# Kernel optimization log

Hardware: AMD Instinct MI355X
Metric: run time of the kernel (lower is better)

## Reference

```python
import jax, jax.numpy as jnp
import numpy as np

B, S, D, H, FFN = 8, 1024, 1024, 16, 4096
DH = D // H  # per-head dim = 64
NEG = -1e9
EPS = 1e-5


def layer_norm(x):
    # F.layer_norm over last dim, no affine params (matches add_and_norm_dropout)
    mu = jnp.mean(x, axis=-1, keepdims=True)
    var = jnp.var(x, axis=-1, keepdims=True)
    return (x - mu) / jnp.sqrt(var + EPS)


def setup_inputs() -> dict:
    key = jax.random.key(0)
    ks = jax.random.split(key, 10)
    scale = 1.0 / np.sqrt(D)
    x = jax.random.normal(ks[0], (B, S, D), dtype=jnp.float32)
    real_lengths = jax.random.randint(ks[1], (B,), 1, S + 1)
    # per-head projection weights stacked: [H, D, DH] (nn.Linear(D, DH, bias=False) per head)
    Wq = jax.random.uniform(ks[2], (H, D, DH), jnp.float32, -scale, scale)
    Wk = jax.random.uniform(ks[3], (H, D, DH), jnp.float32, -scale, scale)
    Wv = jax.random.uniform(ks[4], (H, D, DH), jnp.float32, -scale, scale)
    Wo = jax.random.uniform(ks[5], (D, H * DH), jnp.float32, -scale, scale)  # Linear(H*DH, D, bias=False)
    W1 = jax.random.uniform(ks[6], (FFN, D), jnp.float32, -scale, scale)
    b1 = jax.random.uniform(ks[7], (FFN,), jnp.float32, -scale, scale)
    s2 = 1.0 / np.sqrt(FFN)
    W2 = jax.random.uniform(ks[8], (D, FFN), jnp.float32, -s2, s2)
    b2 = jax.random.uniform(ks[9], (D,), jnp.float32, -s2, s2)
    return {"x": x, "real_lengths": real_lengths, "Wq": Wq, "Wk": Wk, "Wv": Wv,
            "Wo": Wo, "W1": W1, "b1": b1, "W2": W2, "b2": b2}


def reference(x, real_lengths, Wq, Wk, Wv, Wo, W1, b1, W2, b2):
    b, s, d = x.shape
    # padding mask: True where key position >= real_length (masked out)
    key_pad = jnp.arange(s)[None, :] >= real_lengths[:, None]  # [B, S]

    # batched per-head projections (equivalent to the Python per-head loop)
    q = jnp.einsum('bsd,hde->bhse', x, Wq)
    k = jnp.einsum('bsd,hde->bhse', x, Wk)
    v = jnp.einsum('bsd,hde->bhse', x, Wv)

    scores = jnp.einsum('bhse,bhte->bhst', q, k) / jnp.sqrt(jnp.float32(DH))
    scores = jnp.where(key_pad[:, None, None, :], NEG, scores)
    attn = jax.nn.softmax(scores, axis=-1)
    heads = jnp.einsum('bhst,bhte->bhse', attn, v)       # [B,H,S,DH]
    concat = heads.transpose(0, 2, 1, 3).reshape(b, s, d)  # head concat
    attn_out = concat @ Wo.T

    x1 = layer_norm(x + attn_out)  # add & norm (eval: no dropout)

    ffn = jax.nn.relu(x1 @ W1.T + b1) @ W2.T + b2
    return layer_norm(x1 + ffn)
```

## Files before the change

### kernel.cpp

```cpp
#include <hip/hip_runtime.h>
#include <hip/hip_bf16.h>
#include <math.h>

#define B_ 8
#define S_ 1024
#define D_ 1024
#define H_ 16
#define DH_ 64
#define FFN_ 4096
#define NEG_ (-1e9f)
#define EPS_ 1e-5f

typedef float f32x4 __attribute__((ext_vector_type(4)));
typedef short bf16x8 __attribute__((ext_vector_type(8)));

__device__ __forceinline__ ushort f2b(float f) {
  __hip_bfloat16 h = __float2bfloat16(f);
  return *reinterpret_cast<ushort*>(&h);
}
__device__ __forceinline__ float b2f(ushort u) {
  return __uint_as_float((unsigned)u << 16);
}

__device__ __forceinline__ void gload16(const void* g, void* l) {
  auto* lp = (__attribute__((address_space(3))) unsigned*)(uintptr_t)(l);
  __builtin_amdgcn_global_load_lds(
      (const __attribute__((address_space(1))) unsigned*)g, lp, 16, 0, 0);
}

__device__ __forceinline__ void* swz_ptr(void* base, int row, int col) {
  int byte = (row << 7) + (col << 1);
  byte ^= (row & 7) << 4;
  return (char*)base + byte;
}

__global__ __launch_bounds__(256) void prep_k(
    const float* __restrict__ x, const float* __restrict__ Wq,
    const float* __restrict__ Wk, const float* __restrict__ Wv,
    const float* __restrict__ Wo, const float* __restrict__ W1,
    const float* __restrict__ W2, ushort* __restrict__ xbf,
    ushort* __restrict__ qkvw, ushort* __restrict__ wob,
    ushort* __restrict__ w1b, ushort* __restrict__ w2b) {
  const int blk = blockIdx.x, t = threadIdx.x;
  if (blk < 8192) {
    int i = blk * 256 + t;
    float4 v = ((const float4*)x)[i];
    ushort4 o;
    o.x = f2b(v.x); o.y = f2b(v.y); o.z = f2b(v.z); o.w = f2b(v.w);
    ((ushort4*)xbf)[i] = o;
  } else if (blk < 8192 + 12288) {
    int idx = (blk - 8192) * 256 + t;
    int e = idx & 63, k = (idx >> 6) & 1023;
    int h = (idx >> 16) & 15, which = idx >> 20;
    const float* W = (which == 0) ? Wq : (which == 1 ? Wk : Wv);
    float v = W[((size_t)h * D_ + k) * DH_ + e];
    qkvw[((size_t)which * 1024 + h * 64 + e) * 1024 + k] = f2b(v);
  } else if (blk < 8192 + 12288 + 1024) {
    int i = (blk - 8192 - 12288) * 256 + t;
    float4 v = ((const float4*)Wo)[i];
    ushort4 o;
    o.x = f2b(v.x); o.y = f2b(v.y); o.z = f2b(v.z); o.w = f2b(v.w);
    ((ushort4*)wob)[i] = o;
  } else if (blk < 8192 + 12288 + 1024 + 4096) {
    int i = (blk - 8192 - 12288 - 1024) * 256 + t;
    float4 v = ((const float4*)W1)[i];
    ushort4 o;
    o.x = f2b(v.x); o.y = f2b(v.y); o.z = f2b(v.z); o.w = f2b(v.w);
    ((ushort4*)w1b)[i] = o;
  } else {
    int i = (blk - 8192 - 12288 - 1024 - 4096) * 256 + t;
    float4 v = ((const float4*)W2)[i];
    ushort4 o;
    o.x = f2b(v.x); o.y = f2b(v.y); o.z = f2b(v.z); o.w = f2b(v.w);
    ((ushort4*)w2b)[i] = o;
  }
}

template <int BIAS, int RELU, int OUT_BF16, int VSPLIT>
__global__ __launch_bounds__(256) void gemm_bf16(
    const ushort* __restrict__ A, const ushort* __restrict__ Bt,
    const float* __restrict__ bias, void* __restrict__ C,
    ushort* __restrict__ vT, int M, int N, int K) {
  __shared__ ushort Al[2][128 * 64];
  __shared__ ushort Bl[2][128 * 64];
  const int nb = N >> 7;
  const int bm = blockIdx.x / nb, bn = blockIdx.x % nb;
  const int t = threadIdx.x;
  const int lane = t & 63;
  const int wid = t >> 6, wr = wid >> 1, wc = wid & 1;
  const int row0 = bm << 7, col0 = bn << 7;
  const size_t Kb = (size_t)K * 2;
  const int NT = K >> 6;

  const char* Abase = (const char*)A + (size_t)row0 * Kb;
  const char* Bbase = (const char*)Bt + (size_t)col0 * Kb;

  f32x4 acc[4][4] = {};
  const int o0 = t * 16;
  const int lrow = lane & 15, lkb = (lane >> 4) * 8;

  auto STAGE = [&](int buf, int kt) {
#pragma unroll
    for (int i = 0; i < 4; i++) {
      int ob = o0 + i * 4096;
      int row = ob >> 7, inrow = ob & 127;
      const char* ga = Abase + (size_t)row * Kb + kt * 128 + inrow;
      const char* gb = Bbase + (size_t)row * Kb + kt * 128 + inrow;
      gload16(ga, (char*)&Al[buf][0] + ob);
      gload16(gb, (char*)&Bl[buf][0] + ob);
    }
  };
  auto COMPUTE = [&](int buf) {
#pragma unroll
    for (int kk = 0; kk < 64; kk += 32) {
      bf16x8 af[4], bfr[4];
      const int lk = lkb + kk;
#pragma unroll
      for (int m = 0; m < 4; m++)
        af[m] = *(const bf16x8*)&Al[buf][(wr * 64 + m * 16 + lrow) * 64 + lk];
#pragma unroll
      for (int n = 0; n < 4; n++)
        bfr[n] = *(const bf16x8*)&Bl[buf][(wc * 64 + n * 16 + lrow) * 64 + lk];
#pragma unroll
      for (int m = 0; m < 4; m++)
#pragma unroll
        for (int n = 0; n < 4; n++)
          acc[m][n] = __builtin_amdgcn_mfma_f32_16x16x32_bf16(
              af[m], bfr[n], acc[m][n], 0, 0, 0);
    }
  };

  STAGE(0, 0);
  __syncthreads();
  int cur = 0;
  for (int kt = 1; kt < NT; kt++) {
    STAGE(cur ^ 1, kt);
    COMPUTE(cur);
    __syncthreads();
    cur ^= 1;
  }
  COMPUTE(cur);

  const int rbase = row0 + wr * 64 + (lane >> 4) * 4;
  const int cbase = col0 + wc * 64 + (lane & 15);
#pragma unroll
  for (int m = 0; m < 4; m++) {
#pragma unroll
    for (int n = 0; n < 4; n++) {
      int col = cbase + n * 16;
      float bv = BIAS ? bias[col] : 0.0f;
      if (VSPLIT && col >= 2048) {
        int row = rbase + m * 16;
        int hh = (col - 2048) >> 6, e = col & 63;
        ushort4 uv;
        uv.x = f2b(acc[m][n][0]); uv.y = f2b(acc[m][n][1]);
        uv.z = f2b(acc[m][n][2]); uv.w = f2b(acc[m][n][3]);
        *(ushort4*)&vT[((((size_t)(row >> 10) * 16 + hh) * 64 + e) << 10) +
                       (row & 1023)] = uv;
      } else {
#pragma unroll
        for (int q = 0; q < 4; q++) {
          int row = rbase + m * 16 + q;
          float v = acc[m][n][q] + bv;
          if (RELU) v = fmaxf(v, 0.0f);
          if (VSPLIT) {
            ((ushort*)C)[(size_t)row * 2048 + col] = f2b(v);
          } else if (OUT_BF16) {
            ((ushort*)C)[(size_t)row * N + col] = f2b(v);
          } else {
            ((float*)C)[(size_t)row * N + col] = v;
          }
        }
      }
    }
  }
}

__global__ __launch_bounds__(256) void attention_mfma_k(
    const ushort* __restrict__ qk, const ushort* __restrict__ vT,
    const int* __restrict__ lens, ushort* __restrict__ concat) {
  __shared__ ushort Qs[64 * 64];
  __shared__ ushort Ks[64 * 64];
  __shared__ ushort Vt[64 * 64];
  __shared__ ushort Pl[4][16 * 64];
  const int blk = blockIdx.x;
  const int b = blk & 7, h = (blk >> 3) & 15, q0 = (blk >> 7) << 6;
  const int t = threadIdx.x;
  const int lane = t & 63, w = t >> 6;
  const int lr = lane & 15, lg = lane >> 4;
  const int lg4 = lg * 4;
  const int len_b = lens[b];
  ushort* Plw = &Pl[w][0];
  const ushort* vbase = vT + ((size_t)(b * 16 + h) << 16);

#pragma unroll
  for (int i = 0; i < 4; i++) {
    int idx = t + i * 256;
    int r = idx >> 4, eq = idx & 15;
    const ushort* src =
        qk + ((size_t)(b * S_ + q0 + r)) * 2048 + h * 64 + eq * 4;
    *(ushort4*)swz_ptr(Qs, r, eq * 4) = *(const ushort4*)src;
  }
  __syncthreads();
  bf16x8 qf[2];
#pragma unroll
  for (int ds = 0; ds < 2; ds++)
    qf[ds] = *(const bf16x8*)swz_ptr(Qs, w * 16 + lr, lg * 8 + ds * 32);

  float mrun = -INFINITY, lrun = 0.f;
  f32x4 o[4] = {};

  ushort4 kreg[4], vreg[4];
  auto LOADT = [&](int j0) {
#pragma unroll
    for (int i = 0; i < 4; i++) {
      int idx = t + i * 256;
      int r = idx >> 4, eq = idx & 15;
      kreg[i] = *(const ushort4*)(qk + ((size_t)(b * S_ + j0 + r)) * 2048 +
                                  1024 + h * 64 + eq * 4);
      vreg[i] = *(const ushort4*)(vbase + (size_t)r * 1024 + j0 + eq * 4);
    }
  };

  const int ntiles = (len_b + 63) >> 6;
  LOADT(0);
  for (int jt = 0; jt < ntiles; jt++) {
    const int j0 = jt << 6;
    __syncthreads();
#pragma unroll
    for (int i = 0; i < 4; i++) {
      int idx = t + i * 256;
      int r = idx >> 4, eq = idx & 15;
      *(ushort4*)swz_ptr(Ks, r, eq * 4) = kreg[i];
      *(ushort4*)swz_ptr(Vt, r, eq * 4) = vreg[i];
    }
    if (jt + 1 < ntiles) LOADT(j0 + 64);
    __syncthreads();

    f32x4 sacc[4];
    __builtin_amdgcn_s_setprio(1);
#pragma unroll
    for (int mb = 0; mb < 4; mb++) {
      sacc[mb] = (f32x4){0.f, 0.f, 0.f, 0.f};
#pragma unroll
      for (int ds = 0; ds < 2; ds++) {
        bf16x8 kf = *(const bf16x8*)swz_ptr(Ks, mb * 16 + lr, lg * 8 + ds * 32);
        sacc[mb] = __builtin_amdgcn_mfma_f32_16x16x32_bf16(kf, qf[ds], sacc[mb],
                                                           0, 0, 0);
      }
    }
    __builtin_amdgcn_s_setprio(0);

    float p[4][4];
    float pmax = -INFINITY;
#pragma unroll
    for (int mb = 0; mb < 4; mb++)
#pragma unroll
      for (int qi = 0; qi < 4; qi++) {
        float v = sacc[mb][qi] * 0.125f;
        if (j0 + mb * 16 + lg4 + qi >= len_b) v = NEG_;
        p[mb][qi] = v;
        pmax = fmaxf(pmax, v);
      }
    pmax = fmaxf(pmax, __shfl_xor(pmax, 16));
    pmax = fmaxf(pmax, __shfl_xor(pmax, 32));
    if (!__all(pmax - mrun <= 8.0f)) {
      float mnew = fmaxf(mrun, pmax);
      float sc = __expf(mrun - mnew);
      mrun = mnew;
      lrun *= sc;
#pragma unroll
      for (int qi = 0; qi < 4; qi++) {
        float scq = __shfl(sc, (lg << 4) + lg4 + qi);
#pragma unroll
        for (int dt = 0; dt < 4; dt++) o[dt][qi] *= scq;
      }
    }
    float rs = 0.f;
#pragma unroll
    for (int mb = 0; mb < 4; mb++)
#pragma unroll
      for (int qi = 0; qi < 4; qi++) {
        float e = __expf(p[mb][qi] - mrun);
        p[mb][qi] = e;
        rs += e;
      }
    rs += __shfl_xor(rs, 16);
    rs += __shfl_xor(rs, 32);
    lrun += rs;

#pragma unroll
    for (int mb = 0; mb < 4; mb++) {
      ushort2 w0, w1;
      w0.x = f2b(p[mb][0]); w0.y = f2b(p[mb][1]);
      w1.x = f2b(p[mb][2]); w1.y = f2b(p[mb][3]);
      *(ushort2*)swz_ptr(Plw, lr, mb * 16 + lg4) = w0;
      *(ushort2*)swz_ptr(Plw, lr, mb * 16 + lg4 + 2) = w1;
    }

    bf16x8 pf[2];
#pragma unroll
    for (int ks = 0; ks < 2; ks++)
      pf[ks] = *(const bf16x8*)swz_ptr(Plw, lr, lg * 8 + ks * 32);
    __builtin_amdgcn_s_setprio(1);
#pragma unroll
    for (int dt = 0; dt < 4; dt++) {
#pragma unroll
      for (int ks = 0; ks < 2; ks++) {
        bf16x8 vf = *(const bf16x8*)swz_ptr(Vt, dt * 16 + lr, lg * 8 + ks * 32);
        o[dt] = __builtin_amdgcn_mfma_f32_16x16x32_bf16(pf[ks], vf, o[dt],
                                                        0, 0, 0);
      }
    }
    __builtin_amdgcn_s_setprio(0);
  }

#pragma unroll
  for (int qi = 0; qi < 4; qi++) {
    float lq = __shfl(lrun, (lg << 4) + lg4 + qi);
    float inv = 1.0f / lq;
    size_t row = (size_t)(b * S_ + q0 + w * 16 + lg4 + qi);
#pragma unroll
    for (int dt = 0; dt < 4; dt++)
      concat[row * 1024 + h * 64 + dt * 16 + lr] = f2b(o[dt][qi] * inv);
  }
}

template <int WBF>
__global__ __launch_bounds__(256) void add_ln_k(const float* __restrict__ a,
                                                const ushort* __restrict__ r,
                                                float* __restrict__ y,
                                                ushort* __restrict__ yb) {
  const int row = blockIdx.x, t = threadIdx.x;
  const float4 av = ((const float4*)(a + (size_t)row * 1024))[t];
  const ushort4 rv = ((const ushort4*)(r + (size_t)row * 1024))[t];
  float v[4] = {av.x + b2f(rv.x), av.y + b2f(rv.y), av.z + b2f(rv.z),
                av.w + b2f(rv.w)};
  float s = v[0] + v[1] + v[2] + v[3];
  float q = v[0] * v[0] + v[1] * v[1] + v[2] * v[2] + v[3] * v[3];
#pragma unroll
  for (int off = 1; off < 64; off <<= 1) {
    s += __shfl_xor(s, off);
    q += __shfl_xor(q, off);
  }
  __shared__ float ss[4], sq[4];
  int wave = t >> 6, lane = t & 63;
  if (lane == 0) { ss[wave] = s; sq[wave] = q; }
  __syncthreads();
  s = ss[0] + ss[1] + ss[2] + ss[3];
  q = sq[0] + sq[1] + sq[2] + sq[3];
  float mean = s * (1.f / 1024.f);
  float var = q * (1.f / 1024.f) - mean * mean;
  float inv = 1.0f / sqrtf(var + EPS_);
  float4 yo;
  yo.x = (v[0] - mean) * inv; yo.y = (v[1] - mean) * inv;
  yo.z = (v[2] - mean) * inv; yo.w = (v[3] - mean) * inv;
  ((float4*)(y + (size_t)row * 1024))[t] = yo;
  if (WBF) {
    ushort4 ob;
    ob.x = f2b(yo.x); ob.y = f2b(yo.y); ob.z = f2b(yo.z); ob.w = f2b(yo.w);
    ((ushort4*)(yb + (size_t)row * 1024))[t] = ob;
  }
}

extern "C" void kernel_launch(void* const* d_in, const int* in_sizes, int n_in,
                              void* d_out, int out_size, void* d_ws, size_t ws_size,
                              hipStream_t stream) {
  const float* x  = (const float*)d_in[0];
  const int* len  = (const int*)d_in[1];
  const float* Wq = (const float*)d_in[2];
  const float* Wk = (const float*)d_in[3];
  const float* Wv = (const float*)d_in[4];
  const float* Wo = (const float*)d_in[5];
  const float* W1 = (const float*)d_in[6];
  const float* b1 = (const float*)d_in[7];
  const float* W2 = (const float*)d_in[8];
  const float* b2 = (const float*)d_in[9];
  float* out = (float*)d_out;

  if (ws_size < (size_t)184 * 1024 * 1024) return;
  char* w = (char*)d_ws;
  ushort* xbf    = (ushort*)(w);
  ushort* qkvw   = (ushort*)(w + ((size_t)16 << 20));
  ushort* wob    = (ushort*)(w + ((size_t)22 << 20));
  ushort* w1b    = (ushort*)(w + ((size_t)24 << 20));
  ushort* w2b    = (ushort*)(w + ((size_t)32 << 20));
  ushort* qk2    = (ushort*)(w + ((size_t)40 << 20));
  ushort* vT     = (ushort*)(w + ((size_t)72 << 20));
  ushort* concat = (ushort*)(w + ((size_t)88 << 20));
  ushort* attno  = (ushort*)(w + ((size_t)104 << 20));
  float*  x1     = (float*) (w + ((size_t)136 << 20));
  ushort* x1b    = (ushort*)(w + ((size_t)168 << 20));
  ushort* hidden = (ushort*)(w + ((size_t)40 << 20));
  ushort* ffn2o  = (ushort*)(w + ((size_t)104 << 20));

  prep_k<<<29696, 256, 0, stream>>>(x, Wq, Wk, Wv, Wo, W1, W2,
                                    xbf, qkvw, wob, w1b, w2b);

  gemm_bf16<0, 0, 1, 1><<<64 * 24, 256, 0, stream>>>(xbf, qkvw, nullptr, qk2,
                                                     vT, 8192, 3072, 1024);
  attention_mfma_k<<<2048, 256, 0, stream>>>(qk2, vT, len, concat);
  gemm_bf16<0, 0, 1, 0><<<64 * 8, 256, 0, stream>>>(concat, wob, nullptr,
                                                    attno, nullptr,
                                                    8192, 1024, 1024);
  add_ln_k<1><<<8192, 256, 0, stream>>>(x, attno, x1, x1b);
  gemm_bf16<1, 1, 1, 0><<<64 * 32, 256, 0, stream>>>(x1b, w1b, b1, hidden,
                                                     nullptr, 8192, 4096, 1024);
  gemm_bf16<1, 0, 1, 0><<<64 * 8, 256, 0, stream>>>(hidden, w2b, b2, ffn2o,
                                                    nullptr, 8192, 1024, 4096);
  add_ln_k<0><<<8192, 256, 0, stream>>>(x1, ffn2o, out, nullptr);
}
```

Baseline: 404.0 us.

## Add 256x256 8-wave ping-pong GEMM for QKV and FFN1 projections

Adds a new GEMM kernel that uses 256x256 output tiles, 512 threads (8 waves), split-K-half LDS staging with double buffering, explicit barriers and waitcnts, MFMA priority boosting, and an XCD-aware block swizzle. It replaces the old 128x128 kernel for the wide QKV (N=3072) and FFN1 (N=4096) GEMMs, aiming for more data reuse per tile and better overlap of global loads with MFMA work. The old kernel is simplified and kept for the N=1024 GEMMs. The risks are fewer workgroups (384 and 512), which may underfill the CUs, higher register pressure from 32 accumulators per lane, and fragile hand-written synchronisation.

Measured after the change: 386.2 us. 1.05x faster.

```diff
diff --git a/kernel.cpp b/kernel.cpp
--- a/kernel.cpp
+++ b/kernel.cpp
@@ -33,6 +33,13 @@
   byte ^= (row & 7) << 4;
   return (char*)base + byte;
 }
+
+#define BARR asm volatile("s_barrier" ::: "memory")
+#define LGKM0                                         \
+  do {                                                \
+    asm volatile("s_waitcnt lgkmcnt(0)" ::: "memory"); \
+    __builtin_amdgcn_sched_barrier(0);                \
+  } while (0)
 
 __global__ __launch_bounds__(256) void prep_k(
     const float* __restrict__ x, const float* __restrict__ Wq,
@@ -76,11 +83,144 @@
   }
 }
 
-template <int BIAS, int RELU, int OUT_BF16, int VSPLIT>
+template <int BIAS, int RELU, int VSPLIT>
+__global__ __launch_bounds__(512, 2) void gemm8p(
+    const ushort* __restrict__ A, const ushort* __restrict__ Bt,
+    const float* __restrict__ bias, ushort* __restrict__ C,
+    ushort* __restrict__ vT, int M, int N, int K) {
+  __shared__ ushort lds[2][2][2][256 * 32];
+  const int nbn = N >> 8;
+  const int nwg = gridDim.x;
+  const int cpx = nwg >> 3;
+  const int bid = blockIdx.x;
+  const int swz = (bid & 7) * cpx + (bid >> 3);
+  const int bm = swz / nbn, bn = swz % nbn;
+
+  const int t = threadIdx.x;
+  const int lane = t & 63, lr = lane & 15, lg = lane >> 4;
+  const int wid = t >> 6, wr = wid >> 2, wc = wid & 3;
+  const size_t Kb = (size_t)K * 2;
+  const char* Ab = (const char*)A + ((size_t)(bm << 8)) * Kb;
+  const char* Bb = (const char*)Bt + ((size_t)(bn << 8)) * Kb;
+  const int NT = K >> 6;
+  const int niter = NT >> 1;
+
+  const int g0row = t >> 2;
+  const int gsi = (t & 3) ^ (g0row & 3);
+  auto STG = [&](int mat, int kh, int kt) {
+    char* base = (char*)&lds[kt & 1][mat][kh][0];
+    const char* gsrc = mat ? Bb : Ab;
+#pragma unroll
+    for (int j = 0; j < 2; j++) {
+      int row = g0row + j * 128;
+      const char* src = gsrc + (size_t)row * Kb +
+                        (size_t)(kt * 64 + kh * 32) * 2 + gsi * 16;
+      gload16(src, base + t * 16 + j * 8192);
+    }
+  };
+
+  const int rg = (lg ^ (lr & 3)) << 3;
+#define LDA(DST, BUF, KH, QM)                                            \
+  _Pragma("unroll") for (int mm = 0; mm < 4; mm++) {                     \
+    int row = wr * 128 + (QM)*64 + mm * 16 + lr;                         \
+    DST[mm] = *(const bf16x8*)&lds[BUF][0][KH][row * 32 + rg];           \
+  }
+#define LDB(DST, BUF, KH)                                                \
+  _Pragma("unroll") for (int nn = 0; nn < 4; nn++) {                     \
+    int row = wc * 64 + nn * 16 + lr;                                    \
+    DST[nn] = *(const bf16x8*)&lds[BUF][1][KH][row * 32 + rg];           \
+  }
+#define MFQ(QM, AS, BS)                                                  \
+  do {                                                                   \
+    __builtin_amdgcn_s_setprio(1);                                       \
+    _Pragma("unroll") for (int mm = 0; mm < 4; mm++)                     \
+        _Pragma("unroll") for (int nn = 0; nn < 4; nn++)                 \
+            acc[(QM)*4 + mm][nn] = __builtin_amdgcn_mfma_f32_16x16x32_bf16( \
+                AS[mm], BS[nn], acc[(QM)*4 + mm][nn], 0, 0, 0);          \
+    __builtin_amdgcn_s_setprio(0);                                       \
+  } while (0)
+
+  f32x4 acc[8][4] = {};
+  bf16x8 aS0[4], aS1[4], bS0[4], bS1[4];
+
+  STG(0, 0, 0); STG(1, 0, 0); STG(0, 1, 0); STG(1, 1, 0);
+  STG(0, 0, 1); STG(1, 0, 1);
+  asm volatile("s_waitcnt vmcnt(4)" ::: "memory");
+  BARR;
+
+  for (int i = 0; i < niter; i++) {
+    const int c1 = 2 * i + 1, c2 = 2 * i + 2, c3 = 2 * i + 3;
+    LDA(aS0, 0, 0, 0); LDB(bS0, 0, 0); STG(0, 1, c1);
+    BARR; LGKM0; MFQ(0, aS0, bS0); BARR;
+    LDA(aS1, 0, 0, 1); STG(1, 1, c1);
+    BARR; LGKM0; MFQ(1, aS1, bS0); BARR;
+    LDA(aS0, 0, 1, 0); LDB(bS1, 0, 1);
+    if (c2 < NT) STG(0, 0, c2);
+    BARR; LGKM0; MFQ(0, aS0, bS1); BARR;
+    LDA(aS1, 0, 1, 1);
+    if (c2 < NT) STG(1, 0, c2);
+    BARR; LGKM0; MFQ(1, aS1, bS1);
+    if (i + 1 < niter)
+      asm volatile("s_waitcnt vmcnt(4)" ::: "memory");
+    else
+      asm volatile("s_waitcnt vmcnt(0)" ::: "memory");
+    BARR;
+    LDA(aS0, 1, 0, 0); LDB(bS0, 1, 0);
+    if (c2 < NT) STG(0, 1, c2);
+    BARR; LGKM0; MFQ(0, aS0, bS0); BARR;
+    LDA(aS1, 1, 0, 1);
+    if (c2 < NT) STG(1, 1, c2);
+    BARR; LGKM0; MFQ(1, aS1, bS0); BARR;
+    LDA(aS0, 1, 1, 0); LDB(bS1, 1, 1);
+    if (c3 < NT) STG(0, 0, c3);
+    BARR; LGKM0; MFQ(0, aS0, bS1); BARR;
+    LDA(aS1, 1, 1, 1);
+    if (c3 < NT) STG(1, 0, c3);
+    BARR; LGKM0; MFQ(1, aS1, bS1);
+    asm volatile("s_waitcnt vmcnt(4)" ::: "memory");
+    BARR;
+  }
+#undef LDA
+#undef LDB
+#undef MFQ
+
+  const int r0 = (bm << 8) + wr * 128 + lg * 4;
+  const int c0 = (bn << 8) + wc * 64 + lr;
+#pragma unroll
+  for (int m = 0; m < 8; m++) {
+#pragma unroll
+    for (int n = 0; n < 4; n++) {
+      int col = c0 + n * 16;
+      float bv = BIAS ? bias[col] : 0.0f;
+      if (VSPLIT && col >= 2048) {
+        int row = r0 + m * 16;
+        int hh = (col - 2048) >> 6, e = col & 63;
+        ushort4 uv;
+        uv.x = f2b(acc[m][n][0]); uv.y = f2b(acc[m][n][1]);
+        uv.z = f2b(acc[m][n][2]); uv.w = f2b(acc[m][n][3]);
+        *(ushort4*)&vT[((((size_t)(row >> 10) * 16 + hh) * 64 + e) << 10) +
+                       (row & 1023)] = uv;
+      } else {
+#pragma unroll
+        for (int q = 0; q < 4; q++) {
+          int row = r0 + m * 16 + q;
+          float v = acc[m][n][q] + bv;
+          if (RELU) v = fmaxf(v, 0.0f);
+          if (VSPLIT)
+            C[(size_t)row * 2048 + col] = f2b(v);
+          else
+            C[(size_t)row * N + col] = f2b(v);
+        }
+      }
+    }
+  }
+}
+
+template <int BIAS, int RELU>
 __global__ __launch_bounds__(256) void gemm_bf16(
     const ushort* __restrict__ A, const ushort* __restrict__ Bt,
-    const float* __restrict__ bias, void* __restrict__ C,
-    ushort* __restrict__ vT, int M, int N, int K) {
+    const float* __restrict__ bias, ushort* __restrict__ C,
+    int M, int N, int K) {
   __shared__ ushort Al[2][128 * 64];
   __shared__ ushort Bl[2][128 * 64];
   const int nb = N >> 7;
@@ -149,28 +289,12 @@
     for (int n = 0; n < 4; n++) {
       int col = cbase + n * 16;
       float bv = BIAS ? bias[col] : 0.0f;
-      if (VSPLIT && col >= 2048) {
-        int row = rbase + m * 16;
-        int hh = (col - 2048) >> 6, e = col & 63;
-        ushort4 uv;
-        uv.x = f2b(acc[m][n][0]); uv.y = f2b(acc[m][n][1]);
-        uv.z = f2b(acc[m][n][2]); uv.w = f2b(acc[m][n][3]);
-        *(ushort4*)&vT[((((size_t)(row >> 10) * 16 + hh) * 64 + e) << 10) +
-                       (row & 1023)] = uv;
-      } else {
-#pragma unroll
-        for (int q = 0; q < 4; q++) {
-          int row = rbase + m * 16 + q;
-          float v = acc[m][n][q] + bv;
-          if (RELU) v = fmaxf(v, 0.0f);
-          if (VSPLIT) {
-            ((ushort*)C)[(size_t)row * 2048 + col] = f2b(v);
-          } else if (OUT_BF16) {
-            ((ushort*)C)[(size_t)row * N + col] = f2b(v);
-          } else {
-            ((float*)C)[(size_t)row * N + col] = v;
-          }
-        }
+#pragma unroll
+      for (int q = 0; q < 4; q++) {
+        int row = rbase + m * 16 + q;
+        float v = acc[m][n][q] + bv;
+        if (RELU) v = fmaxf(v, 0.0f);
+        C[(size_t)row * N + col] = f2b(v);
       }
     }
   }
@@ -397,16 +521,15 @@
   prep_k<<<29696, 256, 0, stream>>>(x, Wq, Wk, Wv, Wo, W1, W2,
                                     xbf, qkvw, wob, w1b, w2b);
 
-  gemm_bf16<0, 0, 1, 1><<<64 * 24, 256, 0, stream>>>(xbf, qkvw, nullptr, qk2,
-                                                     vT, 8192, 3072, 1024);
+  gemm8p<0, 0, 1><<<32 * 12, 512, 0, stream>>>(xbf, qkvw, nullptr, qk2,
+                                               vT, 8192, 3072, 1024);
   attention_mfma_k<<<2048, 256, 0, stream>>>(qk2, vT, len, concat);
-  gemm_bf16<0, 0, 1, 0><<<64 * 8, 256, 0, stream>>>(concat, wob, nullptr,
-                                                    attno, nullptr,
-                                                    8192, 1024, 1024);
+  gemm_bf16<0, 0><<<64 * 8, 256, 0, stream>>>(concat, wob, nullptr, attno,
+                                              8192, 1024, 1024);
   add_ln_k<1><<<8192, 256, 0, stream>>>(x, attno, x1, x1b);
-  gemm_bf16<1, 1, 1, 0><<<64 * 32, 256, 0, stream>>>(x1b, w1b, b1, hidden,
-                                                     nullptr, 8192, 4096, 1024);
-  gemm_bf16<1, 0, 1, 0><<<64 * 8, 256, 0, stream>>>(hidden, w2b, b2, ffn2o,
-                                                    nullptr, 8192, 1024, 4096);
+  gemm8p<1, 1, 0><<<32 * 16, 512, 0, stream>>>(x1b, w1b, b1, hidden,
+                                               nullptr, 8192, 4096, 1024);
+  gemm_bf16<1, 0><<<64 * 8, 256, 0, stream>>>(hidden, w2b, b2, ffn2o,
+                                              8192, 1024, 4096);
   add_ln_k<0><<<8192, 256, 0, stream>>>(x1, ffn2o, out, nullptr);
 }
```
